# Kernel tuning notes

Measured on AMD Instinct MI355X. Metric: run time of the kernel, lower is better.

The kernel has to match this reference:

```python
import jax, jax.numpy as jnp
import numpy as np
import math

B, T, E, D = 4, 2048, 1024, 4

def _tau_init(t):
    a = 0.1 ** (1.0 / max(t - 1, 1))
    tt = -math.log(max(a, 1e-10))
    return math.log(math.exp(tt) - 1 + 1e-10)

def causal_ema(b, tau_raw):
    # h_t = alpha * h_{t-1} + b_t with alpha = exp(-softplus(tau_raw));
    # exactly equal to the conv1d with kernel exp(-tau*j) in the original.
    alpha = jnp.exp(-jax.nn.softplus(tau_raw)).astype(b.dtype)
    def step(h, bt):
        h = alpha * h + bt
        return h, h
    h0 = jnp.zeros((b.shape[0], b.shape[2]), b.dtype)
    _, hs = jax.lax.scan(step, h0, jnp.swapaxes(b, 0, 1))  # scan over T
    return jnp.swapaxes(hs, 0, 1)

def setup_inputs():
    key = jax.random.key(0)
    ks = jax.random.split(key, 10)
    s = 0.02
    return {
        "x": jax.random.normal(ks[0], (B, T, E), jnp.float32),
        "tau_ctx": jnp.float32(_tau_init(max(T // 2, 4))),
        "tau_raws": jnp.array([_tau_init(max(T // 2 ** i, 2)) for i in range(D)], jnp.float32),
        "Wg": jax.random.normal(ks[1], (E, 2 * E), jnp.float32) * s,
        "bg": jnp.full((E,), -0.5, jnp.float32),
        "Wn1": jax.random.normal(ks[2], (E // 4, E), jnp.float32) * s,
        "bn1": jnp.zeros((E // 4,), jnp.float32),
        "Wn2": jax.random.normal(ks[3], (D, E // 4), jnp.float32) * s,
        "bn2": jnp.zeros((D,), jnp.float32),
        "blend": jax.random.normal(ks[4], (D, E), jnp.float32) * s,
        "Wsoma": jax.random.normal(ks[5], (E, E), jnp.float32) * s,
        "bsoma": jnp.zeros((E,), jnp.float32),
        "Wtemp": jax.random.normal(ks[6], (E, E), jnp.float32) * s,
        "btemp": jnp.zeros((E,), jnp.float32),
        "Wout": jax.random.normal(ks[7], (E, E), jnp.float32) * s,
        "gamma": jnp.ones((E,), jnp.float32),
        "beta": jnp.zeros((E,), jnp.float32),
    }

def reference(x, tau_ctx, tau_raws, Wg, bg, Wn1, bn1, Wn2, bn2, blend, Wsoma, bsoma, Wtemp, btemp, Wout, gamma, beta):
    ctx = causal_ema(x, tau_ctx)                                   # (B,T,E)
    gate_in = jnp.concatenate([x, ctx], axis=-1)                   # (B,T,2E)
    wg = jax.nn.sigmoid(jnp.einsum('btc,ec->bte', gate_in, Wg) + bg)
    gated = x * wg
    h1 = jax.nn.gelu(jnp.einsum('btc,hc->bth', x, Wn1) + bn1, approximate=False)
    mod = 0.5 + jax.nn.sigmoid(jnp.einsum('bth,dh->btd', h1, Wn2) + bn2)  # (B,T,D)
    # neuromod_ema: modulate input then fixed-alpha EMA, one per dendrite
    traces = jax.vmap(lambda tau, m: causal_ema(gated * m[..., None], tau))(
        tau_raws, jnp.moveaxis(mod, -1, 0))                        # (D,B,T,E)
    blend_w = jax.nn.softmax(blend, axis=0)                        # (D,E)
    temporal = jnp.einsum('dbtc,dc->btc', traces, blend_w)
    gate = jax.nn.sigmoid(jnp.einsum('btc,ec->bte', temporal, Wtemp) + btemp)
    soma = jax.nn.gelu(jnp.einsum('btc,ec->bte', x, Wsoma) + bsoma, approximate=False)
    out = jnp.einsum('btc,ec->bte', soma * gate, Wout)
    mu = out.mean(-1, keepdims=True)
    var = out.var(-1, keepdims=True)
    return (out - mu) / jnp.sqrt(var + 1e-5) * gamma + beta
```

## Files before the change

kernel.cpp:

```cpp
#include <hip/hip_runtime.h>
#include <math.h>

#define B_DIM 4
#define T_DIM 2048
#define E_DIM 1024
#define D_DIM 4
#define M_ROWS (B_DIM*T_DIM)
#define NC 16
#define CL (T_DIM/NC)

typedef short short8 __attribute__((ext_vector_type(8)));
typedef float f32x4 __attribute__((ext_vector_type(4)));

__device__ __forceinline__ float bf2f(unsigned short u){
  union { unsigned int i; float f; } c; c.i = ((unsigned int)u) << 16; return c.f;
}
__device__ __forceinline__ unsigned short f2bf(float f){
  union { float f; unsigned int i; } c; c.f = f;
  unsigned int u = c.i;
  return (unsigned short)((u + 0x7FFFu + ((u >> 16) & 1u)) >> 16);
}
__device__ __forceinline__ float sigf(float x){ return 1.f/(1.f+__expf(-x)); }
__device__ __forceinline__ float geluf(float x){ return 0.5f*x*(1.f+erff(x*0.70710678118f)); }

__global__ __launch_bounds__(256) void conv_w_k(const float* __restrict__ s,
                                                unsigned short* __restrict__ d, int n){
  int i = (blockIdx.x*256 + threadIdx.x)*4;
  if (i >= n) return;
  float4 v = *(const float4*)&s[i];
  uint2 p;
  p.x = (unsigned int)f2bf(v.x) | ((unsigned int)f2bf(v.y) << 16);
  p.y = (unsigned int)f2bf(v.z) | ((unsigned int)f2bf(v.w) << 16);
  *(uint2*)&d[i] = p;
}

__global__ __launch_bounds__(256) void conv_x_k(const float* __restrict__ x,
                                                unsigned short* __restrict__ gatein){
  int gid = blockIdx.x*256 + threadIdx.x;
  int idx = gid*4;
  int m = idx >> 10, c = idx & 1023;
  float4 v = *(const float4*)&x[idx];
  uint2 p;
  p.x = (unsigned int)f2bf(v.x) | ((unsigned int)f2bf(v.y) << 16);
  p.y = (unsigned int)f2bf(v.z) | ((unsigned int)f2bf(v.w) << 16);
  *(uint2*)&gatein[(size_t)m*2048 + c] = p;
}

__global__ __launch_bounds__(256) void ctx_carry_k(const float* __restrict__ x,
                                                   const float* __restrict__ tau_ctx,
                                                   float* __restrict__ car){
  int gid = blockIdx.x*256 + threadIdx.x;
  int e = gid & 1023, bc = gid >> 10;
  int b = bc >> 4, chunk = bc & 15;
  float alpha = 1.f/(1.f+expf(tau_ctx[0]));
  const float* xp = x + ((size_t)b*T_DIM + chunk*CL)*E_DIM + e;
  float h = 0.f;
  #pragma unroll 8
  for (int t = 0; t < CL; t++) h = alpha*h + xp[(size_t)t*E_DIM];
  car[(size_t)bc*E_DIM + e] = h;
}

__global__ __launch_bounds__(256) void ctx_scan_k(const float* __restrict__ x,
                                                  const float* __restrict__ tau_ctx,
                                                  const float* __restrict__ car,
                                                  unsigned short* __restrict__ gatein){
  int gid = blockIdx.x*256 + threadIdx.x;
  int e = gid & 1023, bc = gid >> 10;
  int b = bc >> 4, chunk = bc & 15;
  float alpha = 1.f/(1.f+expf(tau_ctx[0]));
  float alphaL = powf(alpha, (float)CL);
  float h = 0.f;
  for (int j = 0; j < chunk; j++) h = alphaL*h + car[(size_t)(b*NC + j)*E_DIM + e];
  const float* xp = x + ((size_t)b*T_DIM + chunk*CL)*E_DIM + e;
  unsigned short* op = gatein + ((size_t)(b*T_DIM + chunk*CL))*2048 + 1024 + e;
  #pragma unroll 8
  for (int t = 0; t < CL; t++){
    h = alpha*h + xp[(size_t)t*E_DIM];
    op[(size_t)t*2048] = f2bf(h);
  }
}

__global__ __launch_bounds__(256) void dend_carry_k(const unsigned short* __restrict__ gated,
                                                    const float* __restrict__ mod,
                                                    const float* __restrict__ tau_raws,
                                                    float* __restrict__ car){
  int gid = blockIdx.x*256 + threadIdx.x;
  int e = gid & 1023, bc = gid >> 10;
  int b = bc >> 4, chunk = bc & 15;
  float a0 = 1.f/(1.f+expf(tau_raws[0]));
  float a1 = 1.f/(1.f+expf(tau_raws[1]));
  float a2 = 1.f/(1.f+expf(tau_raws[2]));
  float a3 = 1.f/(1.f+expf(tau_raws[3]));
  const unsigned short* gp = gated + ((size_t)(b*T_DIM + chunk*CL))*E_DIM + e;
  const float* mp = mod + (size_t)(b*T_DIM + chunk*CL)*4;
  float h0=0.f,h1=0.f,h2=0.f,h3=0.f;
  #pragma unroll 4
  for (int t = 0; t < CL; t++){
    float g = bf2f(gp[(size_t)t*E_DIM]);
    float4 m4 = *(const float4*)&mp[t*4];
    h0 = a0*h0 + g*m4.x; h1 = a1*h1 + g*m4.y; h2 = a2*h2 + g*m4.z; h3 = a3*h3 + g*m4.w;
  }
  size_t base = (size_t)bc*E_DIM + e;
  car[0*65536 + base] = h0; car[1*65536 + base] = h1;
  car[2*65536 + base] = h2; car[3*65536 + base] = h3;
}

__global__ __launch_bounds__(256) void dend_scan_k(const unsigned short* __restrict__ gated,
                                                   const float* __restrict__ mod,
                                                   const float* __restrict__ tau_raws,
                                                   const float* __restrict__ car,
                                                   const float* __restrict__ blend,
                                                   unsigned short* __restrict__ temporal){
  int gid = blockIdx.x*256 + threadIdx.x;
  int e = gid & 1023, bc = gid >> 10;
  int b = bc >> 4, chunk = bc & 15;
  float al[4], hh[4];
  #pragma unroll
  for (int d = 0; d < 4; d++){ al[d] = 1.f/(1.f+expf(tau_raws[d])); hh[d] = 0.f; }
  #pragma unroll
  for (int d = 0; d < 4; d++){
    float aL = powf(al[d], (float)CL);
    float h = 0.f;
    for (int j = 0; j < chunk; j++) h = aL*h + car[(size_t)d*65536 + (size_t)(b*NC + j)*E_DIM + e];
    hh[d] = h;
  }
  float bl[4];
  #pragma unroll
  for (int d = 0; d < 4; d++) bl[d] = blend[d*E_DIM + e];
  float mx = fmaxf(fmaxf(bl[0],bl[1]), fmaxf(bl[2],bl[3]));
  float ex0=__expf(bl[0]-mx), ex1=__expf(bl[1]-mx), ex2=__expf(bl[2]-mx), ex3=__expf(bl[3]-mx);
  float inv = 1.f/(ex0+ex1+ex2+ex3);
  float w0=ex0*inv, w1=ex1*inv, w2=ex2*inv, w3=ex3*inv;

  const unsigned short* gp = gated + ((size_t)(b*T_DIM + chunk*CL))*E_DIM + e;
  const float* mp = mod + (size_t)(b*T_DIM + chunk*CL)*4;
  unsigned short* op = temporal + ((size_t)(b*T_DIM + chunk*CL))*E_DIM + e;
  float h0=hh[0], h1=hh[1], h2=hh[2], h3=hh[3];
  float a0=al[0], a1=al[1], a2=al[2], a3=al[3];
  #pragma unroll 4
  for (int t = 0; t < CL; t++){
    float g = bf2f(gp[(size_t)t*E_DIM]);
    float4 m4 = *(const float4*)&mp[t*4];
    h0 = a0*h0 + g*m4.x; h1 = a1*h1 + g*m4.y; h2 = a2*h2 + g*m4.z; h3 = a3*h3 + g*m4.w;
    float tv = w0*h0 + w1*h1 + w2*h2 + w3*h3;
    op[(size_t)t*E_DIM] = f2bf(tv);
  }
}

__global__ __launch_bounds__(256) void mod_k(const unsigned short* __restrict__ h1,
                                             const float* __restrict__ Wn2,
                                             const float* __restrict__ bn2,
                                             float* __restrict__ mod){
  int wave = threadIdx.x >> 6, lane = threadIdx.x & 63;
  int m = blockIdx.x*4 + wave;
  float p0=0.f,p1=0.f,p2=0.f,p3=0.f;
  for (int c = lane; c < 256; c += 64){
    float h = bf2f(h1[(size_t)m*256 + c]);
    p0 += h*Wn2[0*256 + c]; p1 += h*Wn2[1*256 + c];
    p2 += h*Wn2[2*256 + c]; p3 += h*Wn2[3*256 + c];
  }
  #pragma unroll
  for (int off = 32; off > 0; off >>= 1){
    p0 += __shfl_down(p0, off); p1 += __shfl_down(p1, off);
    p2 += __shfl_down(p2, off); p3 += __shfl_down(p3, off);
  }
  if (lane == 0){
    mod[(size_t)m*4 + 0] = 0.5f + sigf(p0 + bn2[0]);
    mod[(size_t)m*4 + 1] = 0.5f + sigf(p1 + bn2[1]);
    mod[(size_t)m*4 + 2] = 0.5f + sigf(p2 + bn2[2]);
    mod[(size_t)m*4 + 3] = 0.5f + sigf(p3 + bn2[3]);
  }
}

#define BM 128
#define BN 128
#define BK 32

template<int EPI>
__global__ __launch_bounds__(256, 2) void gemm_bf16_k(
    const unsigned short* __restrict__ A, int lda,
    const unsigned short* __restrict__ Bw,
    int K, int N,
    const float* __restrict__ bias,
    const float* __restrict__ xf32,
    const unsigned short* __restrict__ ebf,
    void* __restrict__ outp)
{
  __shared__ unsigned short sA[BM*BK];
  __shared__ unsigned short sB[BN*BK];
  const int tid = threadIdx.x;
  const int row0 = blockIdx.x * BM;
  const int col0 = blockIdx.y * BN;
  const int wave = tid >> 6, lane = tid & 63;
  const int quad = lane >> 4, l15 = lane & 15;
  const int wm = (wave & 1) * 64, wn = (wave >> 1) * 64;

  f32x4 acc[4][4];
  #pragma unroll
  for (int i = 0; i < 4; i++)
    #pragma unroll
    for (int j = 0; j < 4; j++) acc[i][j] = (f32x4){0.f,0.f,0.f,0.f};

  const int r0 = tid >> 2;
  const int r1 = (tid + 256) >> 2;
  const int kc = (tid & 3) * 8;

  for (int k0 = 0; k0 < K; k0 += BK){
    uint4 ga0 = *(const uint4*)&A [(size_t)(row0 + r0)*lda + k0 + kc];
    uint4 ga1 = *(const uint4*)&A [(size_t)(row0 + r1)*lda + k0 + kc];
    uint4 gb0 = *(const uint4*)&Bw[(size_t)(col0 + r0)*K   + k0 + kc];
    uint4 gb1 = *(const uint4*)&Bw[(size_t)(col0 + r1)*K   + k0 + kc];
    __syncthreads();
    *(uint4*)&sA[(size_t)tid*8]       = ga0;
    *(uint4*)&sA[(size_t)(tid+256)*8] = ga1;
    *(uint4*)&sB[(size_t)tid*8]       = gb0;
    *(uint4*)&sB[(size_t)(tid+256)*8] = gb1;
    __syncthreads();
    short8 afr[4], bfr[4];
    #pragma unroll
    for (int i = 0; i < 4; i++) afr[i] = *(const short8*)&sA[(wm + i*16 + l15)*BK + quad*8];
    #pragma unroll
    for (int j = 0; j < 4; j++) bfr[j] = *(const short8*)&sB[(wn + j*16 + l15)*BK + quad*8];
    #pragma unroll
    for (int i = 0; i < 4; i++)
      #pragma unroll
      for (int j = 0; j < 4; j++)
        acc[i][j] = __builtin_amdgcn_mfma_f32_16x16x32_bf16(afr[i], bfr[j], acc[i][j], 0, 0, 0);
  }

  #pragma unroll
  for (int i = 0; i < 4; i++){
    #pragma unroll
    for (int j = 0; j < 4; j++){
      const int col = col0 + wn + j*16 + l15;
      #pragma unroll
      for (int r = 0; r < 4; r++){
        const int row = row0 + wm + i*16 + quad*4 + r;
        float v = acc[i][j][r];
        size_t o = (size_t)row * N + col;
        if (EPI == 0){
          v += bias[col];
          float wg = sigf(v);
          ((unsigned short*)outp)[o] = f2bf(xf32[o] * wg);
        } else if (EPI == 1){
          v += bias[col];
          ((unsigned short*)outp)[o] = f2bf(geluf(v));
        } else if (EPI == 2){
          v += bias[col];
          ((unsigned short*)outp)[o] = f2bf(sigf(v) * bf2f(ebf[o]));
        } else {
          ((float*)outp)[o] = v;
        }
      }
    }
  }
}

__global__ __launch_bounds__(256) void ln_k(const float* __restrict__ in,
                                            const float* __restrict__ gamma,
                                            const float* __restrict__ beta,
                                            float* __restrict__ out){
  __shared__ float s1[4], s2[4];
  int row = blockIdx.x, tid = threadIdx.x;
  float4 v = *(const float4*)&in[(size_t)row*1024 + tid*4];
  float s = v.x+v.y+v.z+v.w;
  float q = v.x*v.x+v.y*v.y+v.z*v.z+v.w*v.w;
  #pragma unroll
  for (int off = 32; off > 0; off >>= 1){ s += __shfl_down(s, off); q += __shfl_down(q, off); }
  int wave = tid >> 6, lane = tid & 63;
  if (lane == 0){ s1[wave] = s; s2[wave] = q; }
  __syncthreads();
  s = s1[0]+s1[1]+s1[2]+s1[3];
  q = s2[0]+s2[1]+s2[2]+s2[3];
  float mu = s*(1.f/1024.f);
  float var = q*(1.f/1024.f) - mu*mu;
  float rs = rsqrtf(var + 1e-5f);
  int c = tid*4;
  float4 g = *(const float4*)&gamma[c];
  float4 bb = *(const float4*)&beta[c];
  float4 o;
  o.x = (v.x-mu)*rs*g.x + bb.x;
  o.y = (v.y-mu)*rs*g.y + bb.y;
  o.z = (v.z-mu)*rs*g.z + bb.z;
  o.w = (v.w-mu)*rs*g.w + bb.w;
  *(float4*)&out[(size_t)row*1024 + c] = o;
}

extern "C" void kernel_launch(void* const* d_in, const int* in_sizes, int n_in,
                              void* d_out, int out_size, void* d_ws, size_t ws_size,
                              hipStream_t stream) {
  const float* x        = (const float*)d_in[0];
  const float* tau_ctx  = (const float*)d_in[1];
  const float* tau_raws = (const float*)d_in[2];
  const float* Wg       = (const float*)d_in[3];
  const float* bg       = (const float*)d_in[4];
  const float* Wn1      = (const float*)d_in[5];
  const float* bn1      = (const float*)d_in[6];
  const float* Wn2      = (const float*)d_in[7];
  const float* bn2      = (const float*)d_in[8];
  const float* blend    = (const float*)d_in[9];
  const float* Wsoma    = (const float*)d_in[10];
  const float* bsoma    = (const float*)d_in[11];
  const float* Wtemp    = (const float*)d_in[12];
  const float* btemp    = (const float*)d_in[13];
  const float* Wout     = (const float*)d_in[14];
  const float* gamma    = (const float*)d_in[15];
  const float* beta     = (const float*)d_in[16];

  char* ws = (char*)d_ws;
  unsigned short* gatein   = (unsigned short*)(ws + 0);
  float*          out_pre  = (float*)(ws + 0);
  unsigned short* wg_bf    = (unsigned short*)(ws + 33554432);
  unsigned short* wn1_bf   = (unsigned short*)(ws + 37748736);
  unsigned short* wsoma_bf = (unsigned short*)(ws + 38273024);
  unsigned short* wtemp_bf = (unsigned short*)(ws + 40370176);
  unsigned short* wout_bf  = (unsigned short*)(ws + 42467328);
  unsigned short* h1_bf    = (unsigned short*)(ws + 44564480);
  float*          modbuf   = (float*)(ws + 48758784);
  float*          car_ctx  = (float*)(ws + 48889856);
  float*          car_d    = (float*)(ws + 49152000);
  unsigned short* gated    = (unsigned short*)(ws + 50200576);
  unsigned short* sg       = gated;
  unsigned short* temporal = (unsigned short*)(ws + 66977792);
  unsigned short* soma     = (unsigned short*)(ws + 83755008);

  conv_x_k<<<dim3(M_ROWS*E_DIM/4/256), dim3(256), 0, stream>>>(x, gatein);
  conv_w_k<<<dim3(2048), dim3(256), 0, stream>>>(Wg,    wg_bf,    2097152);
  conv_w_k<<<dim3(256),  dim3(256), 0, stream>>>(Wn1,   wn1_bf,   262144);
  conv_w_k<<<dim3(1024), dim3(256), 0, stream>>>(Wsoma, wsoma_bf, 1048576);
  conv_w_k<<<dim3(1024), dim3(256), 0, stream>>>(Wtemp, wtemp_bf, 1048576);
  conv_w_k<<<dim3(1024), dim3(256), 0, stream>>>(Wout,  wout_bf,  1048576);

  ctx_carry_k<<<dim3(256), dim3(256), 0, stream>>>(x, tau_ctx, car_ctx);
  ctx_scan_k <<<dim3(256), dim3(256), 0, stream>>>(x, tau_ctx, car_ctx, gatein);

  gemm_bf16_k<0><<<dim3(M_ROWS/BM, 1024/BN), dim3(256), 0, stream>>>(
      gatein, 2048, wg_bf, 2048, 1024, bg, x, nullptr, gated);

  gemm_bf16_k<1><<<dim3(M_ROWS/BM, 256/BN), dim3(256), 0, stream>>>(
      gatein, 2048, wn1_bf, 1024, 256, bn1, nullptr, nullptr, h1_bf);

  mod_k<<<dim3(M_ROWS/4), dim3(256), 0, stream>>>(h1_bf, Wn2, bn2, modbuf);

  dend_carry_k<<<dim3(256), dim3(256), 0, stream>>>(gated, modbuf, tau_raws, car_d);
  dend_scan_k <<<dim3(256), dim3(256), 0, stream>>>(gated, modbuf, tau_raws, car_d, blend, temporal);

  gemm_bf16_k<1><<<dim3(M_ROWS/BM, 1024/BN), dim3(256), 0, stream>>>(
      gatein, 2048, wsoma_bf, 1024, 1024, bsoma, nullptr, nullptr, soma);

  gemm_bf16_k<2><<<dim3(M_ROWS/BM, 1024/BN), dim3(256), 0, stream>>>(
      temporal, 1024, wtemp_bf, 1024, 1024, btemp, nullptr, soma, sg);

  gemm_bf16_k<3><<<dim3(M_ROWS/BM, 1024/BN), dim3(256), 0, stream>>>(
      sg, 1024, wout_bf, 1024, 1024, nullptr, nullptr, nullptr, out_pre);

  ln_k<<<dim3(M_ROWS), dim3(256), 0, stream>>>(out_pre, gamma, beta, (float*)d_out);
}
```

Measured before the change: 390.4 us.

## Fuse conversions, merge soma/Wn1 GEMMs, vectorize scans, use direct global-to-LDS loads

Folds the separate weight-conversion launches into a single kernel and writes the bf16 copy of x inside the context scan, so the standalone x conversion pass goes away. The soma and Wn1 GEMMs become one wider GEMM over concatenated weights and biases, with outputs split in the epilogue. The scan kernels double the chunk count and have each thread handle two channels with vectorized loads and stores. The GEMM stages tiles through global_load_lds instead of register staging. This cuts launches, memory passes and register traffic, at the cost of reworked workspace aliasing that must stay correct.

```diff
diff --git a/kernel.cpp b/kernel.cpp
--- a/kernel.cpp
+++ b/kernel.cpp
@@ -4,9 +4,8 @@
 #define B_DIM 4
 #define T_DIM 2048
 #define E_DIM 1024
-#define D_DIM 4
 #define M_ROWS (B_DIM*T_DIM)
-#define NC 16
+#define NC 32
 #define CL (T_DIM/NC)
 
 typedef short short8 __attribute__((ext_vector_type(8)));
@@ -20,44 +19,59 @@
   unsigned int u = c.i;
   return (unsigned short)((u + 0x7FFFu + ((u >> 16) & 1u)) >> 16);
 }
+__device__ __forceinline__ unsigned int pack2(float a, float b){
+  return (unsigned int)f2bf(a) | ((unsigned int)f2bf(b) << 16);
+}
 __device__ __forceinline__ float sigf(float x){ return 1.f/(1.f+__expf(-x)); }
 __device__ __forceinline__ float geluf(float x){ return 0.5f*x*(1.f+erff(x*0.70710678118f)); }
 
-__global__ __launch_bounds__(256) void conv_w_k(const float* __restrict__ s,
-                                                unsigned short* __restrict__ d, int n){
-  int i = (blockIdx.x*256 + threadIdx.x)*4;
-  if (i >= n) return;
-  float4 v = *(const float4*)&s[i];
-  uint2 p;
-  p.x = (unsigned int)f2bf(v.x) | ((unsigned int)f2bf(v.y) << 16);
-  p.y = (unsigned int)f2bf(v.z) | ((unsigned int)f2bf(v.w) << 16);
-  *(uint2*)&d[i] = p;
-}
-
-__global__ __launch_bounds__(256) void conv_x_k(const float* __restrict__ x,
-                                                unsigned short* __restrict__ gatein){
-  int gid = blockIdx.x*256 + threadIdx.x;
-  int idx = gid*4;
-  int m = idx >> 10, c = idx & 1023;
-  float4 v = *(const float4*)&x[idx];
-  uint2 p;
-  p.x = (unsigned int)f2bf(v.x) | ((unsigned int)f2bf(v.y) << 16);
-  p.y = (unsigned int)f2bf(v.z) | ((unsigned int)f2bf(v.w) << 16);
-  *(uint2*)&gatein[(size_t)m*2048 + c] = p;
+__device__ __forceinline__ void glds16(const unsigned short* g, unsigned short* l){
+  __builtin_amdgcn_global_load_lds((const __attribute__((address_space(1))) void*)g,
+                                   (__attribute__((address_space(3))) void*)l, 16, 0, 0);
+}
+
+__device__ __forceinline__ void cvt4(const float* __restrict__ s, unsigned short* __restrict__ d){
+  float4 v = *(const float4*)s;
+  uint2 p; p.x = pack2(v.x, v.y); p.y = pack2(v.z, v.w);
+  *(uint2*)d = p;
+}
+
+__global__ __launch_bounds__(256) void conv_all_k(
+    const float* __restrict__ Wg, const float* __restrict__ Wsoma,
+    const float* __restrict__ Wn1, const float* __restrict__ Wtemp,
+    const float* __restrict__ Wout, const float* __restrict__ bsoma,
+    const float* __restrict__ bn1,
+    unsigned short* __restrict__ wg_bf, unsigned short* __restrict__ wsn1,
+    unsigned short* __restrict__ wtemp_bf, unsigned short* __restrict__ wout_bf,
+    float* __restrict__ bsn1){
+  int u = blockIdx.x*256 + threadIdx.x;
+  if (u < 524288){ cvt4(Wg + (size_t)u*4, wg_bf + (size_t)u*4); }
+  else if (u < 786432){ u -= 524288; cvt4(Wsoma + (size_t)u*4, wsn1 + (size_t)u*4); }
+  else if (u < 851968){ u -= 786432; cvt4(Wn1 + (size_t)u*4, wsn1 + 1048576 + (size_t)u*4); }
+  else if (u < 1114112){ u -= 851968; cvt4(Wtemp + (size_t)u*4, wtemp_bf + (size_t)u*4); }
+  else if (u < 1376256){ u -= 1114112; cvt4(Wout + (size_t)u*4, wout_bf + (size_t)u*4); }
+  else if (u < 1376576){
+    u -= 1376256; int i = u*4;
+    float4 v = (i < 1024) ? *(const float4*)&bsoma[i] : *(const float4*)&bn1[i-1024];
+    *(float4*)&bsn1[i] = v;
+  }
 }
 
 __global__ __launch_bounds__(256) void ctx_carry_k(const float* __restrict__ x,
                                                    const float* __restrict__ tau_ctx,
                                                    float* __restrict__ car){
   int gid = blockIdx.x*256 + threadIdx.x;
-  int e = gid & 1023, bc = gid >> 10;
-  int b = bc >> 4, chunk = bc & 15;
+  int e2 = (gid & 511)*2, bc = gid >> 9;
+  int b = bc >> 5, chunk = bc & 31;
   float alpha = 1.f/(1.f+expf(tau_ctx[0]));
-  const float* xp = x + ((size_t)b*T_DIM + chunk*CL)*E_DIM + e;
-  float h = 0.f;
+  const float2* xp = (const float2*)(x + ((size_t)b*T_DIM + chunk*CL)*E_DIM + e2);
+  float h0 = 0.f, h1 = 0.f;
   #pragma unroll 8
-  for (int t = 0; t < CL; t++) h = alpha*h + xp[(size_t)t*E_DIM];
-  car[(size_t)bc*E_DIM + e] = h;
+  for (int t = 0; t < CL; t++){
+    float2 v = xp[(size_t)t*512];
+    h0 = alpha*h0 + v.x; h1 = alpha*h1 + v.y;
+  }
+  *(float2*)&car[(size_t)bc*E_DIM + e2] = make_float2(h0, h1);
 }
 
 __global__ __launch_bounds__(256) void ctx_scan_k(const float* __restrict__ x,
@@ -65,18 +79,23 @@
                                                   const float* __restrict__ car,
                                                   unsigned short* __restrict__ gatein){
   int gid = blockIdx.x*256 + threadIdx.x;
-  int e = gid & 1023, bc = gid >> 10;
-  int b = bc >> 4, chunk = bc & 15;
+  int e2 = (gid & 511)*2, bc = gid >> 9;
+  int b = bc >> 5, chunk = bc & 31;
   float alpha = 1.f/(1.f+expf(tau_ctx[0]));
   float alphaL = powf(alpha, (float)CL);
-  float h = 0.f;
-  for (int j = 0; j < chunk; j++) h = alphaL*h + car[(size_t)(b*NC + j)*E_DIM + e];
-  const float* xp = x + ((size_t)b*T_DIM + chunk*CL)*E_DIM + e;
-  unsigned short* op = gatein + ((size_t)(b*T_DIM + chunk*CL))*2048 + 1024 + e;
-  #pragma unroll 8
+  float h0 = 0.f, h1 = 0.f;
+  for (int j = 0; j < chunk; j++){
+    float2 c = *(const float2*)&car[(size_t)(b*NC + j)*E_DIM + e2];
+    h0 = alphaL*h0 + c.x; h1 = alphaL*h1 + c.y;
+  }
+  const float2* xp = (const float2*)(x + ((size_t)b*T_DIM + chunk*CL)*E_DIM + e2);
+  unsigned int* op = (unsigned int*)(gatein + ((size_t)(b*T_DIM + chunk*CL))*2048 + e2);
+  #pragma unroll 4
   for (int t = 0; t < CL; t++){
-    h = alpha*h + xp[(size_t)t*E_DIM];
-    op[(size_t)t*2048] = f2bf(h);
+    float2 v = xp[(size_t)t*512];
+    h0 = alpha*h0 + v.x; h1 = alpha*h1 + v.y;
+    op[(size_t)t*1024]       = pack2(v.x, v.y);
+    op[(size_t)t*1024 + 512] = pack2(h0, h1);
   }
 }
 
@@ -85,24 +104,27 @@
                                                     const float* __restrict__ tau_raws,
                                                     float* __restrict__ car){
   int gid = blockIdx.x*256 + threadIdx.x;
-  int e = gid & 1023, bc = gid >> 10;
-  int b = bc >> 4, chunk = bc & 15;
-  float a0 = 1.f/(1.f+expf(tau_raws[0]));
-  float a1 = 1.f/(1.f+expf(tau_raws[1]));
-  float a2 = 1.f/(1.f+expf(tau_raws[2]));
-  float a3 = 1.f/(1.f+expf(tau_raws[3]));
-  const unsigned short* gp = gated + ((size_t)(b*T_DIM + chunk*CL))*E_DIM + e;
-  const float* mp = mod + (size_t)(b*T_DIM + chunk*CL)*4;
-  float h0=0.f,h1=0.f,h2=0.f,h3=0.f;
+  int e2 = (gid & 511)*2, bc = gid >> 9;
+  int b = bc >> 5, chunk = bc & 31;
+  float a[4];
+  #pragma unroll
+  for (int d = 0; d < 4; d++) a[d] = 1.f/(1.f+expf(tau_raws[d]));
+  const ushort2* gp = (const ushort2*)(gated + ((size_t)(b*T_DIM + chunk*CL))*E_DIM + e2);
+  const float4* mp = (const float4*)(mod + (size_t)(b*T_DIM + chunk*CL)*4);
+  float hx[4] = {0,0,0,0}, hy[4] = {0,0,0,0};
   #pragma unroll 4
   for (int t = 0; t < CL; t++){
-    float g = bf2f(gp[(size_t)t*E_DIM]);
-    float4 m4 = *(const float4*)&mp[t*4];
-    h0 = a0*h0 + g*m4.x; h1 = a1*h1 + g*m4.y; h2 = a2*h2 + g*m4.z; h3 = a3*h3 + g*m4.w;
-  }
-  size_t base = (size_t)bc*E_DIM + e;
-  car[0*65536 + base] = h0; car[1*65536 + base] = h1;
-  car[2*65536 + base] = h2; car[3*65536 + base] = h3;
+    ushort2 gv = gp[(size_t)t*512];
+    float gx = bf2f(gv.x), gy = bf2f(gv.y);
+    float4 m4 = mp[t];
+    hx[0] = a[0]*hx[0] + gx*m4.x; hy[0] = a[0]*hy[0] + gy*m4.x;
+    hx[1] = a[1]*hx[1] + gx*m4.y; hy[1] = a[1]*hy[1] + gy*m4.y;
+    hx[2] = a[2]*hx[2] + gx*m4.z; hy[2] = a[2]*hy[2] + gy*m4.z;
+    hx[3] = a[3]*hx[3] + gx*m4.w; hy[3] = a[3]*hy[3] + gy*m4.w;
+  }
+  #pragma unroll
+  for (int d = 0; d < 4; d++)
+    *(float2*)&car[(size_t)d*131072 + (size_t)bc*E_DIM + e2] = make_float2(hx[d], hy[d]);
 }
 
 __global__ __launch_bounds__(256) void dend_scan_k(const unsigned short* __restrict__ gated,
@@ -112,38 +134,52 @@
                                                    const float* __restrict__ blend,
                                                    unsigned short* __restrict__ temporal){
   int gid = blockIdx.x*256 + threadIdx.x;
-  int e = gid & 1023, bc = gid >> 10;
-  int b = bc >> 4, chunk = bc & 15;
-  float al[4], hh[4];
-  #pragma unroll
-  for (int d = 0; d < 4; d++){ al[d] = 1.f/(1.f+expf(tau_raws[d])); hh[d] = 0.f; }
+  int e2 = (gid & 511)*2, bc = gid >> 9;
+  int b = bc >> 5, chunk = bc & 31;
+  float a[4], hx[4], hy[4];
+  #pragma unroll
+  for (int d = 0; d < 4; d++) a[d] = 1.f/(1.f+expf(tau_raws[d]));
   #pragma unroll
   for (int d = 0; d < 4; d++){
-    float aL = powf(al[d], (float)CL);
-    float h = 0.f;
-    for (int j = 0; j < chunk; j++) h = aL*h + car[(size_t)d*65536 + (size_t)(b*NC + j)*E_DIM + e];
-    hh[d] = h;
-  }
-  float bl[4];
-  #pragma unroll
-  for (int d = 0; d < 4; d++) bl[d] = blend[d*E_DIM + e];
-  float mx = fmaxf(fmaxf(bl[0],bl[1]), fmaxf(bl[2],bl[3]));
-  float ex0=__expf(bl[0]-mx), ex1=__expf(bl[1]-mx), ex2=__expf(bl[2]-mx), ex3=__expf(bl[3]-mx);
-  float inv = 1.f/(ex0+ex1+ex2+ex3);
-  float w0=ex0*inv, w1=ex1*inv, w2=ex2*inv, w3=ex3*inv;
-
-  const unsigned short* gp = gated + ((size_t)(b*T_DIM + chunk*CL))*E_DIM + e;
-  const float* mp = mod + (size_t)(b*T_DIM + chunk*CL)*4;
-  unsigned short* op = temporal + ((size_t)(b*T_DIM + chunk*CL))*E_DIM + e;
-  float h0=hh[0], h1=hh[1], h2=hh[2], h3=hh[3];
-  float a0=al[0], a1=al[1], a2=al[2], a3=al[3];
+    float aL = powf(a[d], (float)CL);
+    float h0 = 0.f, h1 = 0.f;
+    for (int j = 0; j < chunk; j++){
+      float2 c = *(const float2*)&car[(size_t)d*131072 + (size_t)(b*NC + j)*E_DIM + e2];
+      h0 = aL*h0 + c.x; h1 = aL*h1 + c.y;
+    }
+    hx[d] = h0; hy[d] = h1;
+  }
+  float blx[4], bly[4];
+  #pragma unroll
+  for (int d = 0; d < 4; d++){
+    float2 bl = *(const float2*)&blend[(size_t)d*E_DIM + e2];
+    blx[d] = bl.x; bly[d] = bl.y;
+  }
+  float mxx = fmaxf(fmaxf(blx[0],blx[1]), fmaxf(blx[2],blx[3]));
+  float mxy = fmaxf(fmaxf(bly[0],bly[1]), fmaxf(bly[2],bly[3]));
+  float wx[4], wy[4], sx = 0.f, sy = 0.f;
+  #pragma unroll
+  for (int d = 0; d < 4; d++){ wx[d] = __expf(blx[d]-mxx); sx += wx[d];
+                               wy[d] = __expf(bly[d]-mxy); sy += wy[d]; }
+  float ix = 1.f/sx, iy = 1.f/sy;
+  #pragma unroll
+  for (int d = 0; d < 4; d++){ wx[d] *= ix; wy[d] *= iy; }
+
+  const ushort2* gp = (const ushort2*)(gated + ((size_t)(b*T_DIM + chunk*CL))*E_DIM + e2);
+  const float4* mp = (const float4*)(mod + (size_t)(b*T_DIM + chunk*CL)*4);
+  unsigned int* op = (unsigned int*)(temporal + ((size_t)(b*T_DIM + chunk*CL))*E_DIM + e2);
   #pragma unroll 4
   for (int t = 0; t < CL; t++){
-    float g = bf2f(gp[(size_t)t*E_DIM]);
-    float4 m4 = *(const float4*)&mp[t*4];
-    h0 = a0*h0 + g*m4.x; h1 = a1*h1 + g*m4.y; h2 = a2*h2 + g*m4.z; h3 = a3*h3 + g*m4.w;
-    float tv = w0*h0 + w1*h1 + w2*h2 + w3*h3;
-    op[(size_t)t*E_DIM] = f2bf(tv);
+    ushort2 gv = gp[(size_t)t*512];
+    float gx = bf2f(gv.x), gy = bf2f(gv.y);
+    float4 m4 = mp[t];
+    hx[0] = a[0]*hx[0] + gx*m4.x; hy[0] = a[0]*hy[0] + gy*m4.x;
+    hx[1] = a[1]*hx[1] + gx*m4.y; hy[1] = a[1]*hy[1] + gy*m4.y;
+    hx[2] = a[2]*hx[2] + gx*m4.z; hy[2] = a[2]*hy[2] + gy*m4.z;
+    hx[3] = a[3]*hx[3] + gx*m4.w; hy[3] = a[3]*hy[3] + gy*m4.w;
+    float tvx = wx[0]*hx[0] + wx[1]*hx[1] + wx[2]*hx[2] + wx[3]*hx[3];
+    float tvy = wy[0]*hy[0] + wy[1]*hy[1] + wy[2]*hy[2] + wy[3]*hy[3];
+    op[(size_t)t*512] = pack2(tvx, tvy);
   }
 }
 
@@ -172,28 +208,32 @@
   }
 }
 
-#define BM 128
-#define BN 128
-#define BK 32
-
 template<int EPI>
-__global__ __launch_bounds__(256, 2) void gemm_bf16_k(
+__global__ __launch_bounds__(256, 2) void gemm_k(
     const unsigned short* __restrict__ A, int lda,
-    const unsigned short* __restrict__ Bw,
-    int K, int N,
+    const unsigned short* __restrict__ Bw, int K,
     const float* __restrict__ bias,
     const float* __restrict__ xf32,
     const unsigned short* __restrict__ ebf,
-    void* __restrict__ outp)
+    void* __restrict__ outp, void* __restrict__ outp2)
 {
-  __shared__ unsigned short sA[BM*BK];
-  __shared__ unsigned short sB[BN*BK];
+  __shared__ unsigned short sA[128*32];
+  __shared__ unsigned short sB[128*32];
   const int tid = threadIdx.x;
-  const int row0 = blockIdx.x * BM;
-  const int col0 = blockIdx.y * BN;
-  const int wave = tid >> 6, lane = tid & 63;
+  const int wv = tid >> 6, lane = tid & 63;
   const int quad = lane >> 4, l15 = lane & 15;
-  const int wm = (wave & 1) * 64, wn = (wave >> 1) * 64;
+  const int wm = (wv & 1) * 64, wn = (wv >> 1) * 64;
+  const int row0 = blockIdx.x * 128, col0 = blockIdx.y * 128;
+
+  const int r = tid >> 2, kc = (tid & 3) * 8;
+  const unsigned short* pa0 = A  + (size_t)(row0 + r)*lda      + kc;
+  const unsigned short* pa1 = A  + (size_t)(row0 + 64 + r)*lda + kc;
+  const unsigned short* pb0 = Bw + (size_t)(col0 + r)*K        + kc;
+  const unsigned short* pb1 = Bw + (size_t)(col0 + 64 + r)*K   + kc;
+  unsigned short* la0 = &sA[wv*512];
+  unsigned short* la1 = &sA[2048 + wv*512];
+  unsigned short* lb0 = &sB[wv*512];
+  unsigned short* lb1 = &sB[2048 + wv*512];
 
   f32x4 acc[4][4];
   #pragma unroll
@@ -201,26 +241,18 @@
     #pragma unroll
     for (int j = 0; j < 4; j++) acc[i][j] = (f32x4){0.f,0.f,0.f,0.f};
 
-  const int r0 = tid >> 2;
-  const int r1 = (tid + 256) >> 2;
-  const int kc = (tid & 3) * 8;
-
-  for (int k0 = 0; k0 < K; k0 += BK){
-    uint4 ga0 = *(const uint4*)&A [(size_t)(row0 + r0)*lda + k0 + kc];
-    uint4 ga1 = *(const uint4*)&A [(size_t)(row0 + r1)*lda + k0 + kc];
-    uint4 gb0 = *(const uint4*)&Bw[(size_t)(col0 + r0)*K   + k0 + kc];
-    uint4 gb1 = *(const uint4*)&Bw[(size_t)(col0 + r1)*K   + k0 + kc];
+  for (int k0 = 0; k0 < K; k0 += 32){
     __syncthreads();
-    *(uint4*)&sA[(size_t)tid*8]       = ga0;
-    *(uint4*)&sA[(size_t)(tid+256)*8] = ga1;
-    *(uint4*)&sB[(size_t)tid*8]       = gb0;
-    *(uint4*)&sB[(size_t)(tid+256)*8] = gb1;
+    glds16(pa0 + k0, la0);
+    glds16(pa1 + k0, la1);
+    glds16(pb0 + k0, lb0);
+    glds16(pb1 + k0, lb1);
     __syncthreads();
     short8 afr[4], bfr[4];
     #pragma unroll
-    for (int i = 0; i < 4; i++) afr[i] = *(const short8*)&sA[(wm + i*16 + l15)*BK + quad*8];
-    #pragma unroll
-    for (int j = 0; j < 4; j++) bfr[j] = *(const short8*)&sB[(wn + j*16 + l15)*BK + quad*8];
+    for (int i = 0; i < 4; i++) afr[i] = *(const short8*)&sA[(wm + i*16 + l15)*32 + quad*8];
+    #pragma unroll
+    for (int j = 0; j < 4; j++) bfr[j] = *(const short8*)&sB[(wn + j*16 + l15)*32 + quad*8];
     #pragma unroll
     for (int i = 0; i < 4; i++)
       #pragma unroll
@@ -234,22 +266,24 @@
     for (int j = 0; j < 4; j++){
       const int col = col0 + wn + j*16 + l15;
       #pragma unroll
-      for (int r = 0; r < 4; r++){
-        const int row = row0 + wm + i*16 + quad*4 + r;
-        float v = acc[i][j][r];
-        size_t o = (size_t)row * N + col;
+      for (int rr = 0; rr < 4; rr++){
+        const int row = row0 + wm + i*16 + quad*4 + rr;
+        float v = acc[i][j][rr];
         if (EPI == 0){
+          size_t o = (size_t)row*1024 + col;
           v += bias[col];
-          float wg = sigf(v);
-          ((unsigned short*)outp)[o] = f2bf(xf32[o] * wg);
+          ((unsigned short*)outp)[o] = f2bf(xf32[o] * sigf(v));
         } else if (EPI == 1){
           v += bias[col];
-          ((unsigned short*)outp)[o] = f2bf(geluf(v));
+          float g = geluf(v);
+          if (col < 1024) ((unsigned short*)outp )[(size_t)row*1024 + col]        = f2bf(g);
+          else            ((unsigned short*)outp2)[(size_t)row*256  + (col-1024)] = f2bf(g);
         } else if (EPI == 2){
+          size_t o = (size_t)row*1024 + col;
           v += bias[col];
           ((unsigned short*)outp)[o] = f2bf(sigf(v) * bf2f(ebf[o]));
         } else {
-          ((float*)outp)[o] = v;
+          ((float*)outp)[(size_t)row*1024 + col] = v;
         }
       }
     }
@@ -311,48 +345,41 @@
   unsigned short* gatein   = (unsigned short*)(ws + 0);
   float*          out_pre  = (float*)(ws + 0);
   unsigned short* wg_bf    = (unsigned short*)(ws + 33554432);
-  unsigned short* wn1_bf   = (unsigned short*)(ws + 37748736);
-  unsigned short* wsoma_bf = (unsigned short*)(ws + 38273024);
+  unsigned short* wsn1     = (unsigned short*)(ws + 37748736);
   unsigned short* wtemp_bf = (unsigned short*)(ws + 40370176);
   unsigned short* wout_bf  = (unsigned short*)(ws + 42467328);
-  unsigned short* h1_bf    = (unsigned short*)(ws + 44564480);
-  float*          modbuf   = (float*)(ws + 48758784);
-  float*          car_ctx  = (float*)(ws + 48889856);
-  float*          car_d    = (float*)(ws + 49152000);
-  unsigned short* gated    = (unsigned short*)(ws + 50200576);
+  float*          bsn1     = (float*)(ws + 44564480);
+  unsigned short* h1_bf    = (unsigned short*)(ws + 44572672);
+  float*          car_d    = (float*)(ws + 44572672);
+  float*          car_ctx  = (float*)(ws + 48766976);
+  float*          modbuf   = (float*)(ws + 48766976);
+  unsigned short* gated    = (unsigned short*)(ws + 49291264);
   unsigned short* sg       = gated;
-  unsigned short* temporal = (unsigned short*)(ws + 66977792);
-  unsigned short* soma     = (unsigned short*)(ws + 83755008);
-
-  conv_x_k<<<dim3(M_ROWS*E_DIM/4/256), dim3(256), 0, stream>>>(x, gatein);
-  conv_w_k<<<dim3(2048), dim3(256), 0, stream>>>(Wg,    wg_bf,    2097152);
-  conv_w_k<<<dim3(256),  dim3(256), 0, stream>>>(Wn1,   wn1_bf,   262144);
-  conv_w_k<<<dim3(1024), dim3(256), 0, stream>>>(Wsoma, wsoma_bf, 1048576);
-  conv_w_k<<<dim3(1024), dim3(256), 0, stream>>>(Wtemp, wtemp_bf, 1048576);
-  conv_w_k<<<dim3(1024), dim3(256), 0, stream>>>(Wout,  wout_bf,  1048576);
+  unsigned short* temporal = (unsigned short*)(ws + 66068480);
+  unsigned short* soma     = (unsigned short*)(ws + 82845696);
+
+  conv_all_k<<<dim3(5378), dim3(256), 0, stream>>>(Wg, Wsoma, Wn1, Wtemp, Wout, bsoma, bn1,
+                                                   wg_bf, wsn1, wtemp_bf, wout_bf, bsn1);
 
   ctx_carry_k<<<dim3(256), dim3(256), 0, stream>>>(x, tau_ctx, car_ctx);
   ctx_scan_k <<<dim3(256), dim3(256), 0, stream>>>(x, tau_ctx, car_ctx, gatein);
 
-  gemm_bf16_k<0><<<dim3(M_ROWS/BM, 1024/BN), dim3(256), 0, stream>>>(
-      gatein, 2048, wg_bf, 2048, 1024, bg, x, nullptr, gated);
-
-  gemm_bf16_k<1><<<dim3(M_ROWS/BM, 256/BN), dim3(256), 0, stream>>>(
-      gatein, 2048, wn1_bf, 1024, 256, bn1, nullptr, nullptr, h1_bf);
+  gemm_k<0><<<dim3(64, 8), dim3(256), 0, stream>>>(
+      gatein, 2048, wg_bf, 2048, bg, x, nullptr, gated, nullptr);
+
+  gemm_k<1><<<dim3(64, 10), dim3(256), 0, stream>>>(
+      gatein, 2048, wsn1, 1024, bsn1, nullptr, nullptr, soma, h1_bf);
 
   mod_k<<<dim3(M_ROWS/4), dim3(256), 0, stream>>>(h1_bf, Wn2, bn2, modbuf);
 
   dend_carry_k<<<dim3(256), dim3(256), 0, stream>>>(gated, modbuf, tau_raws, car_d);
   dend_scan_k <<<dim3(256), dim3(256), 0, stream>>>(gated, modbuf, tau_raws, car_d, blend, temporal);
 
-  gemm_bf16_k<1><<<dim3(M_ROWS/BM, 1024/BN), dim3(256), 0, stream>>>(
-      gatein, 2048, wsoma_bf, 1024, 1024, bsoma, nullptr, nullptr, soma);
-
-  gemm_bf16_k<2><<<dim3(M_ROWS/BM, 1024/BN), dim3(256), 0, stream>>>(
-      temporal, 1024, wtemp_bf, 1024, 1024, btemp, nullptr, soma, sg);
-
-  gemm_bf16_k<3><<<dim3(M_ROWS/BM, 1024/BN), dim3(256), 0, stream>>>(
-      sg, 1024, wout_bf, 1024, 1024, nullptr, nullptr, nullptr, out_pre);
+  gemm_k<2><<<dim3(64, 8), dim3(256), 0, stream>>>(
+      temporal, 1024, wtemp_bf, 1024, btemp, nullptr, soma, sg, nullptr);
+
+  gemm_k<3><<<dim3(64, 8), dim3(256), 0, stream>>>(
+      sg, 1024, wout_bf, 1024, nullptr, nullptr, nullptr, out_pre, nullptr);
 
   ln_k<<<dim3(M_ROWS), dim3(256), 0, stream>>>(out_pre, gamma, beta, (float*)d_out);
 }
```

After: 387.0 us. Within noise of the previous version (-0.9%).
